# Performance work log

Hardware: AMD Instinct MI355X
Metric: run time of the kernel (lower is better)

## Reference

```python
import jax, jax.numpy as jnp
import numpy as np

B, DX, DY, K, H = 131072, 256, 32, 4, 128
TIMESTEPS = 1000
LR, REG, SW = 0.1, 0.01, 1.0


def setup_inputs() -> dict:
    key = jax.random.key(0)
    ks = jax.random.split(key, 12)
    n = lambda k, shp, s=0.05: (jax.random.normal(k, shp) * s).astype(jnp.float32)
    return {
        "x": jax.random.normal(ks[0], (B, DX), jnp.float32),
        "t": jax.random.randint(ks[1], (B,), 0, K),
        "e_w1": n(ks[2], (DX + DY, H)), "e_b1": jnp.zeros((H,), jnp.float32),
        "e_w2": n(ks[3], (H, H)),       "e_b2": jnp.zeros((H,), jnp.float32),
        "e_w3": n(ks[4], (H, K)),       "e_b3": jnp.zeros((K,), jnp.float32),
        "s_xw": n(ks[5], (DX, H)),      "s_xb": jnp.zeros((H,), jnp.float32),
        "s_yw": n(ks[6], (DY, H)),      "s_yb": jnp.zeros((H,), jnp.float32),
        "s_temb": n(ks[7], (K, H)),
        "s_t1w": n(ks[8], (1, H)),      "s_t1b": jnp.zeros((H,), jnp.float32),
        "s_t2w": n(ks[9], (H, H)),      "s_t2b": jnp.zeros((H,), jnp.float32),
        "tr1w": n(ks[10], (4 * H, H)),  "tr1b": jnp.zeros((H,), jnp.float32),
        "tr2w": n(ks[11], (H, K)),      "tr2b": jnp.zeros((K,), jnp.float32),
        "steps": 20,
    }


def reference(x, t, e_w1, e_b1, e_w2, e_b2, e_w3, e_b3,
              s_xw, s_xb, s_yw, s_yb, s_temb, s_t1w, s_t1b, s_t2w, s_t2b,
              tr1w, tr1b, tr2w, tr2b, steps):
    tc = jnp.maximum(t, 0)                      # clamp_min(0)
    tci = tc[:, None]                           # [B,1] gather index
    valid = (t >= 0).astype(jnp.float32)[:, None]
    tau = jnp.maximum(tc.astype(jnp.float32) / TIMESTEPS, 1e-6)[:, None]  # [B,1]

    # y-independent precomputations (hoisted out of the loop)
    hx_e = x @ e_w1[:DX] + e_b1                 # energy first layer, x part [B,H]
    hx_s = x @ s_xw + s_xb                      # score x_proj [B,H]
    temb = s_temb[tc]                           # t embedding [B,H]
    th = jax.nn.silu(tau @ s_t1w + s_t1b) @ s_t2w + s_t2b  # time_fc [B,H]

    def total_fn(y):
        # EnergyNet: Linear-ReLU-Linear-ReLU-Linear on cat([x,y])
        h1 = jax.nn.relu(hx_e + y @ e_w1[DX:])
        e_all = jax.nn.relu(h1 @ e_w2 + e_b2) @ e_w3 + e_b3          # [B,K]
        e = jnp.take_along_axis(e_all, tci, axis=1)                  # [B,1]
        tot = e + REG * jnp.sum(y * y, axis=1, keepdims=True)
        # ScoreNet trunk on cat([x_proj, y_proj, t_embed, time_fc])
        hy = y @ s_yw + s_yb
        h = jnp.concatenate([hx_s, hy, temb, th], axis=-1)           # [B,4H]
        logits = jax.nn.silu(h @ tr1w + tr1b) @ tr2w + tr2b          # [B,K]
        ce = jax.nn.logsumexp(logits, axis=-1, keepdims=True) - jnp.take_along_axis(logits, tci, axis=1)
        return jnp.sum(tot + SW * ce * valid)

    grad_fn = jax.grad(total_fn)

    def step(carry, _):
        y, done = carry
        g = grad_fn(y)
        done = done | (jnp.sqrt(jnp.sum(g * g)) < 1e-3)  # torch: break before update
        y = jnp.where(done, y, y - LR * g)
        return (y, done), None

    y0 = jnp.zeros((x.shape[0], DY), jnp.float32)
    (y, _), _ = jax.lax.scan(step, (y0, jnp.array(False)), None, length=steps)
    return y
```

## Files before the change

kernel.cpp:

```cpp
#include <hip/hip_runtime.h>
#include <hip/hip_bf16.h>

#define DXc 256
#define DYc 32
#define Kc 4
#define Hc 128
#define LRf 0.1f
#define REGf 0.01f
#define TSTEPS 1000

typedef __attribute__((ext_vector_type(8))) short s8b;
typedef __attribute__((ext_vector_type(4))) float f32x4;

#define MFMA16(a, b, c) __builtin_amdgcn_mfma_f32_16x16x32_bf16((a), (b), (c), 0, 0, 0)

#define MFMA6(A0, A1, A2, B0, B1, B2, acc)      \
    do {                                        \
        acc = MFMA16((A0), (B0), acc);          \
        acc = MFMA16((A0), (B1), acc);          \
        acc = MFMA16((A1), (B0), acc);          \
        acc = MFMA16((A0), (B2), acc);          \
        acc = MFMA16((A1), (B1), acc);          \
        acc = MFMA16((A2), (B0), acc);          \
    } while (0)

__device__ __forceinline__ float hipart(float a) {
    return __uint_as_float(__float_as_uint(a) & 0xffff0000u);
}
__device__ __forceinline__ unsigned hi2(float a, float b) {
    return (__float_as_uint(a) >> 16) | (__float_as_uint(b) & 0xffff0000u);
}
__device__ __forceinline__ void wsplit(float x, unsigned short* __restrict__ h,
                                       unsigned short* __restrict__ l) {
    unsigned u = __float_as_uint(x);
    *h = (unsigned short)(u >> 16);
    float hf = __uint_as_float(u & 0xffff0000u);
    *l = (unsigned short)(__float_as_uint(x - hf) >> 16);
}
__device__ __forceinline__ void wsplit3(float x, unsigned short* __restrict__ p0,
                                        unsigned short* __restrict__ p1,
                                        unsigned short* __restrict__ p2) {
    unsigned u = __float_as_uint(x);
    *p0 = (unsigned short)(u >> 16);
    float r1 = x - __uint_as_float(u & 0xffff0000u);
    unsigned u1 = __float_as_uint(r1);
    *p1 = (unsigned short)(u1 >> 16);
    float r2 = r1 - __uint_as_float(u1 & 0xffff0000u);
    *p2 = (unsigned short)(__float_as_uint(r2) >> 16);
}
__device__ __forceinline__ void split3x8(const float* v, s8b& A0, s8b& A1, s8b& A2) {
    union { s8b s; unsigned u[4]; } P0, P1, P2;
    #pragma unroll
    for (int m = 0; m < 4; ++m) {
        float a = v[2 * m], b = v[2 * m + 1];
        unsigned ua = __float_as_uint(a), ub = __float_as_uint(b);
        P0.u[m] = (ua >> 16) | (ub & 0xffff0000u);
        float ra = a - __uint_as_float(ua & 0xffff0000u);
        float rb = b - __uint_as_float(ub & 0xffff0000u);
        unsigned ura = __float_as_uint(ra), urb = __float_as_uint(rb);
        P1.u[m] = (ura >> 16) | (urb & 0xffff0000u);
        float ra2 = ra - __uint_as_float(ura & 0xffff0000u);
        float rb2 = rb - __uint_as_float(urb & 0xffff0000u);
        P2.u[m] = (__float_as_uint(ra2) >> 16) | (__float_as_uint(rb2) & 0xffff0000u);
    }
    A0 = P0.s; A1 = P1.s; A2 = P2.s;
}
__device__ __forceinline__ void split3pack4(const float* v, uint2& Q0, uint2& Q1, uint2& Q2) {
    float r1[4], r2[4];
    #pragma unroll
    for (int i = 0; i < 4; ++i) {
        r1[i] = v[i] - hipart(v[i]);
        r2[i] = r1[i] - hipart(r1[i]);
    }
    Q0.x = hi2(v[0], v[1]);   Q0.y = hi2(v[2], v[3]);
    Q1.x = hi2(r1[0], r1[1]); Q1.y = hi2(r1[2], r1[3]);
    Q2.x = hi2(r2[0], r2[1]); Q2.y = hi2(r2[2], r2[3]);
}
__device__ __forceinline__ void split2pack4(const float* v, uint2& Q0, uint2& Q1) {
    Q0.x = hi2(v[0], v[1]); Q0.y = hi2(v[2], v[3]);
    float r0 = v[0] - hipart(v[0]), r1 = v[1] - hipart(v[1]);
    float r2 = v[2] - hipart(v[2]), r3 = v[3] - hipart(v[3]);
    Q1.x = hi2(r0, r1); Q1.y = hi2(r2, r3);
}

__global__ __launch_bounds__(256) void setup_kernel(
    const float* __restrict__ e_w1, const float* __restrict__ s_xw,
    const float* __restrict__ s_yw, const float* __restrict__ s_temb,
    const float* __restrict__ s_t1w, const float* __restrict__ s_t1b,
    const float* __restrict__ s_t2w, const float* __restrict__ s_t2b,
    const float* __restrict__ tr1w, const float* __restrict__ tr1b,
    const float* __restrict__ s_xb, const float* __restrict__ s_yb,
    const float* __restrict__ e_w2,
    float* __restrict__ Wcat, float* __restrict__ W1, float* __restrict__ d0,
    unsigned short* __restrict__ W1Tb0, unsigned short* __restrict__ W1Tb1,
    unsigned short* __restrict__ W1Tb2,
    unsigned short* __restrict__ ew2Tb0, unsigned short* __restrict__ ew2Tb1,
    unsigned short* __restrict__ ew2Tb2,
    unsigned short* __restrict__ ew2bh, unsigned short* __restrict__ ew2bl,
    unsigned short* __restrict__ Wdybh, unsigned short* __restrict__ Wdybl)
{
    const int b = blockIdx.x;
    const int t = threadIdx.x;
    if (b < 64) {
        #pragma unroll
        for (int i = 0; i < 2; ++i) {
            int idx = t + 256 * i;
            int k = 4 * b + (idx >> 7);
            int c = idx & 127;
            float acc = 0.f;
            for (int h = 0; h < 128; ++h)
                acc += s_xw[k * 128 + h] * tr1w[h * 128 + c];
            Wcat[k * 256 + 128 + c] = acc;
            Wcat[k * 256 + c] = e_w1[k * 128 + c];
        }
    } else if (b == 64) {
        #pragma unroll
        for (int i = 0; i < 16; ++i) {
            int idx = t + 256 * i;
            int d = idx >> 7, c = idx & 127;
            float acc = 0.f;
            for (int h = 0; h < 128; ++h)
                acc += s_yw[d * 128 + h] * tr1w[(128 + h) * 128 + c];
            W1[d * 256 + 128 + c] = acc;
            wsplit3(acc, &W1Tb0[(128 + c) * 32 + d], &W1Tb1[(128 + c) * 32 + d],
                    &W1Tb2[(128 + c) * 32 + d]);
            wsplit(acc, &Wdybh[d * 256 + c], &Wdybl[d * 256 + c]);
        }
    } else if (b == 65) {
        #pragma unroll
        for (int i = 0; i < 16; ++i) {
            int idx = t + 256 * i;
            int d = idx >> 7, c = idx & 127;
            float v = e_w1[(DXc + d) * 128 + c];
            W1[d * 256 + c] = v;
            wsplit3(v, &W1Tb0[c * 32 + d], &W1Tb1[c * 32 + d], &W1Tb2[c * 32 + d]);
            wsplit(v, &Wdybh[d * 256 + 128 + c], &Wdybl[d * 256 + 128 + c]);
        }
    } else if (b == 66) {
        #pragma unroll
        for (int i = 0; i < 64; ++i) {
            int idx = t + 256 * i;
            int h = idx >> 7, c = idx & 127;
            float v = e_w2[h * 128 + c];
            wsplit3(v, &ew2Tb0[c * 128 + h], &ew2Tb1[c * 128 + h],
                    &ew2Tb2[c * 128 + h]);
            wsplit(v, &ew2bh[h * 128 + c], &ew2bl[h * 128 + c]);
        }
    } else {
        __shared__ float thS[4][128];
        #pragma unroll
        for (int i = 0; i < 2; ++i) {
            int idx = t + 256 * i;
            int tt = idx >> 7, c = idx & 127;
            float tau = (float)tt / (float)TSTEPS;
            if (tau < 1e-6f) tau = 1e-6f;
            float acc = s_t2b[c];
            for (int h = 0; h < 128; ++h) {
                float aa = tau * s_t1w[h] + s_t1b[h];
                float s = 1.f / (1.f + expf(-aa));
                acc += aa * s * s_t2w[h * 128 + c];
            }
            thS[tt][c] = acc;
        }
        __syncthreads();
        #pragma unroll
        for (int i = 0; i < 2; ++i) {
            int idx = t + 256 * i;
            int tt = idx >> 7, c = idx & 127;
            float acc = tr1b[c];
            for (int h = 0; h < 128; ++h) {
                acc += s_temb[tt * 128 + h] * tr1w[(256 + h) * 128 + c];
                acc += thS[tt][h]           * tr1w[(384 + h) * 128 + c];
                acc += s_yb[h]              * tr1w[(128 + h) * 128 + c];
                acc += s_xb[h]              * tr1w[h * 128 + c];
            }
            d0[tt * 128 + c] = acc;
        }
    }
}

__global__ __launch_bounds__(256) void rowpre_kernel(
    const float* __restrict__ x, const int* __restrict__ tin,
    const float* __restrict__ Wcat, const float* __restrict__ e_b1,
    const float* __restrict__ d0,
    float* __restrict__ hxeP, float* __restrict__ cbP)
{
    __shared__ float XsT[64][68];
    __shared__ int tS[64];
    __shared__ float eb1S[128];

    const int t = threadIdx.x;
    const int r0 = blockIdx.x * 64;
    if (t < 64) { int tv = tin[r0 + t]; tS[t] = tv > 0 ? tv : 0; }
    if (t < 128) eb1S[t] = e_b1[t];

    const int rg = t >> 4;
    const int cg = t & 15;
    const int R = rg << 2;

    float acc[4][16];
    #pragma unroll
    for (int rr = 0; rr < 4; ++rr)
        #pragma unroll
        for (int cc = 0; cc < 16; ++cc) acc[rr][cc] = 0.f;

    for (int kc = 0; kc < 4; ++kc) {
        __syncthreads();
        #pragma unroll
        for (int i = 0; i < 4; ++i) {
            int lin = t + 256 * i;
            int rr = lin >> 4;
            int c4 = (lin & 15) << 2;
            float4 v = *(const float4*)&x[(size_t)(r0 + rr) * 256 + kc * 64 + c4];
            XsT[c4 + 0][rr] = v.x;
            XsT[c4 + 1][rr] = v.y;
            XsT[c4 + 2][rr] = v.z;
            XsT[c4 + 3][rr] = v.w;
        }
        __syncthreads();
        #pragma unroll 2
        for (int k = 0; k < 64; ++k) {
            float av[4];
            #pragma unroll
            for (int rr = 0; rr < 4; ++rr) av[rr] = XsT[k][R + rr];
            const float* wrow = &Wcat[(size_t)(kc * 64 + k) * 256 + cg];
            #pragma unroll
            for (int cc = 0; cc < 16; ++cc) {
                float bv = wrow[cc * 16];
                #pragma unroll
                for (int rr = 0; rr < 4; ++rr) acc[rr][cc] += av[rr] * bv;
            }
        }
    }
    #pragma unroll
    for (int cc = 0; cc < 8; ++cc) {
        int c = cg + (cc << 4);
        #pragma unroll
        for (int rr = 0; rr < 4; ++rr)
            hxeP[(size_t)(r0 + R + rr) * 128 + c] = acc[rr][cc] + eb1S[c];
    }
    #pragma unroll
    for (int cc = 8; cc < 16; ++cc) {
        int c = cg + ((cc - 8) << 4);
        #pragma unroll
        for (int rr = 0; rr < 4; ++rr)
            cbP[(size_t)(r0 + R + rr) * 128 + c] = acc[rr][cc] + d0[tS[R + rr] * 128 + c];
    }
}

__global__ __launch_bounds__(256) void iterate_kernel(
    const float* __restrict__ hxeP, const float* __restrict__ cbP,
    const unsigned short* __restrict__ W1Tb0, const unsigned short* __restrict__ W1Tb1,
    const unsigned short* __restrict__ W1Tb2,
    const unsigned short* __restrict__ ew2Tb0, const unsigned short* __restrict__ ew2Tb1,
    const unsigned short* __restrict__ ew2Tb2,
    const unsigned short* __restrict__ ew2bh, const unsigned short* __restrict__ ew2bl,
    const unsigned short* __restrict__ Wdybh, const unsigned short* __restrict__ Wdybl,
    const float* __restrict__ e_w3, const float* __restrict__ tr2w,
    const float* __restrict__ tr2b, const float* __restrict__ e_b2,
    const int* __restrict__ tin, const int* __restrict__ stepsPtr,
    float* __restrict__ yout)
{
    __shared__ __align__(16) unsigned short H1a[32 * 136];
    __shared__ __align__(16) unsigned short H1b[32 * 136];
    __shared__ __align__(16) unsigned short H1c[32 * 136];
    __shared__ __align__(16) unsigned short DAa[32 * 136], DAb[32 * 136];
    __shared__ __align__(16) float U[32 * 140];
    __shared__ __align__(16) float yS[32 * 36];
    __shared__ __align__(16) float tr2wS[2 * 520];
    __shared__ float ew3S[512];
    __shared__ float eb2S[128];
    __shared__ float vSs[32];
    __shared__ int tcS[32];

    const int t = threadIdx.x;
    const int r0 = blockIdx.x * 32;
    const int w = t >> 6;
    const int l = t & 63;
    const int g = l >> 4;
    const int q = l & 15;

    if (t < 32) {
        int tv = tin[r0 + t];
        tcS[t] = tv > 0 ? tv : 0;
        vSs[t] = (tv >= 0) ? 1.f : 0.f;
    }
    if (t < 128) eb2S[t] = e_b2[t];
    for (int i = t; i < 512; i += 256) {
        float wv = tr2w[i];
        ew3S[i] = e_w3[i];
        tr2wS[i] = wv;
        tr2wS[520 + i] = wv;
    }
    for (int i = t; i < 32 * 36; i += 256) yS[i] = 0.f;

    float4 vhc4[4][2];
    {
        const float* src = (w < 2) ? hxeP : cbP;
        const int wb = (w < 2) ? w : (w - 2);
        #pragma unroll
        for (int ci = 0; ci < 4; ++ci)
            #pragma unroll
            for (int ct = 0; ct < 2; ++ct)
                vhc4[ci][ct] = *(const float4*)
                    &src[(size_t)(r0 + ct * 16 + q) * 128 + (wb * 4 + ci) * 16 + g * 4];
    }

    s8b W1A0[4], W1A1[4], W1A2[4];
    #pragma unroll
    for (int ci = 0; ci < 4; ++ci) {
        const int arow = (w * 4 + ci) * 16 + q;
        W1A0[ci] = *(const s8b*)&W1Tb0[arow * 32 + g * 8];
        W1A1[ci] = *(const s8b*)&W1Tb1[arow * 32 + g * 8];
        W1A2[ci] = *(const s8b*)&W1Tb2[arow * 32 + g * 8];
    }

    const float tb0 = tr2b[0], tb1 = tr2b[1], tb2 = tr2b[2], tb3 = tr2b[3];
    const int nsteps = stepsPtr[0];
    const int row8 = t >> 3;
    const int p = t & 7;

    __syncthreads();

    for (int step = 0; step < nsteps; ++step) {
        #pragma unroll
        for (int ct = 0; ct < 2; ++ct) {
            float4 ya = *(const float4*)&yS[(ct * 16 + q) * 36 + g * 8];
            float4 yb = *(const float4*)&yS[(ct * 16 + q) * 36 + g * 8 + 4];
            float yv[8] = {ya.x, ya.y, ya.z, ya.w, yb.x, yb.y, yb.z, yb.w};
            s8b Y0, Y1, Y2;
            split3x8(yv, Y0, Y1, Y2);
            #pragma unroll
            for (int ci = 0; ci < 4; ++ci) {
                f32x4 acc = {0.f, 0.f, 0.f, 0.f};
                MFMA6(W1A0[ci], W1A1[ci], W1A2[ci], Y0, Y1, Y2, acc);
                const float4 vb = vhc4[ci][ct];
                if (w < 2) {
                    float v[4];
                    v[0] = acc[0] + vb.x; v[1] = acc[1] + vb.y;
                    v[2] = acc[2] + vb.z; v[3] = acc[3] + vb.w;
                    #pragma unroll
                    for (int j = 0; j < 4; ++j) v[j] = v[j] > 0.f ? v[j] : 0.f;
                    uint2 Q0, Q1, Q2;
                    split3pack4(v, Q0, Q1, Q2);
                    const int off = (ct * 16 + q) * 136 + (w * 4 + ci) * 16 + g * 4;
                    *(uint2*)&H1a[off] = Q0;
                    *(uint2*)&H1b[off] = Q1;
                    *(uint2*)&H1c[off] = Q2;
                } else {
                    float4 o;
                    o.x = acc[0] + vb.x; o.y = acc[1] + vb.y;
                    o.z = acc[2] + vb.z; o.w = acc[3] + vb.w;
                    const int off = (ct * 16 + q) * 140 + ((w - 2) * 4 + ci) * 16 + g * 4;
                    *(float4*)&U[off] = o;
                }
            }
        }
        __syncthreads();

        {
            float aval[16], sval[16];
            float lg0 = 0.f, lg1 = 0.f, lg2 = 0.f, lg3 = 0.f;
            const int h0 = p << 4;
            const float* ap = &U[row8 * 140 + h0];
            #pragma unroll
            for (int m = 0; m < 4; ++m) {
                float4 v4 = *(const float4*)&ap[m * 4];
                aval[m * 4 + 0] = v4.x; aval[m * 4 + 1] = v4.y;
                aval[m * 4 + 2] = v4.z; aval[m * 4 + 3] = v4.w;
            }
            const float* tw = &tr2wS[(p & 1) * 520];
            #pragma unroll
            for (int hh = 0; hh < 16; ++hh) {
                float a = aval[hh];
                float s = 1.f / (1.f + __expf(-a));
                sval[hh] = s;
                float u = a * s;
                float4 wv4 = *(const float4*)&tw[(h0 + hh) * 4];
                lg0 += u * wv4.x; lg1 += u * wv4.y;
                lg2 += u * wv4.z; lg3 += u * wv4.w;
            }
            #pragma unroll
            for (int m = 1; m < 8; m <<= 1) {
                lg0 += __shfl_xor(lg0, m);
                lg1 += __shfl_xor(lg1, m);
                lg2 += __shfl_xor(lg2, m);
                lg3 += __shfl_xor(lg3, m);
            }
            lg0 += tb0; lg1 += tb1; lg2 += tb2; lg3 += tb3;
            float mx = fmaxf(fmaxf(lg0, lg1), fmaxf(lg2, lg3));
            float e0 = __expf(lg0 - mx), e1 = __expf(lg1 - mx);
            float e2 = __expf(lg2 - mx), e3 = __expf(lg3 - mx);
            float inv = 1.f / (e0 + e1 + e2 + e3);
            int tcr = tcS[row8];
            float vd = vSs[row8];
            float dl0 = (e0 * inv - (tcr == 0 ? 1.f : 0.f)) * vd;
            float dl1 = (e1 * inv - (tcr == 1 ? 1.f : 0.f)) * vd;
            float dl2 = (e2 * inv - (tcr == 2 ? 1.f : 0.f)) * vd;
            float dl3 = (e3 * inv - (tcr == 3 ? 1.f : 0.f)) * vd;
            #pragma unroll
            for (int hh = 0; hh < 16; ++hh) {
                float a = aval[hh], s = sval[hh];
                float4 wv4 = *(const float4*)&tw[(h0 + hh) * 4];
                float du = dl0 * wv4.x + dl1 * wv4.y + dl2 * wv4.z + dl3 * wv4.w;
                aval[hh] = du * s * (1.f + a * (1.f - s));
            }
            #pragma unroll
            for (int m = 0; m < 8; ++m) {
                float a0 = aval[2 * m], a1 = aval[2 * m + 1];
                *(unsigned*)&DAa[row8 * 136 + h0 + 2 * m] = hi2(a0, a1);
                *(unsigned*)&DAb[row8 * 136 + h0 + 2 * m] =
                    hi2(a0 - hipart(a0), a1 - hipart(a1));
            }
        }
        __syncthreads();

        {
            unsigned short* DZh = (unsigned short*)U;
            unsigned short* DZl = DZh + 32 * 136;
            #pragma unroll
            for (int ct = 0; ct < 2; ++ct) {
                s8b Ba[4], Bb[4], Bc[4];
                #pragma unroll
                for (int kc = 0; kc < 4; ++kc) {
                    const int off = (ct * 16 + q) * 136 + kc * 32 + g * 8;
                    Ba[kc] = *(const s8b*)&H1a[off];
                    Bb[kc] = *(const s8b*)&H1b[off];
                    Bc[kc] = *(const s8b*)&H1c[off];
                }
                #pragma unroll
                for (int c2 = 0; c2 < 2; ++c2) {
                    const int ctl = w * 2 + c2;
                    f32x4 acc = {0.f, 0.f, 0.f, 0.f};
                    #pragma unroll
                    for (int kc = 0; kc < 4; ++kc) {
                        const int wo = (ctl * 16 + q) * 128 + kc * 32 + g * 8;
                        s8b A0 = *(const s8b*)&ew2Tb0[wo];
                        s8b A1 = *(const s8b*)&ew2Tb1[wo];
                        s8b A2 = *(const s8b*)&ew2Tb2[wo];
                        MFMA6(A0, A1, A2, Ba[kc], Bb[kc], Bc[kc], acc);
                    }
                    const int cb = ctl * 16 + g * 4;
                    const int smp = ct * 16 + q;
                    const float4 eb = *(const float4*)&eb2S[cb];
                    const int tcr = tcS[smp];
                    float dz[4];
                    dz[0] = (acc[0] + eb.x) > 0.f ? ew3S[(cb + 0) * 4 + tcr] : 0.f;
                    dz[1] = (acc[1] + eb.y) > 0.f ? ew3S[(cb + 1) * 4 + tcr] : 0.f;
                    dz[2] = (acc[2] + eb.z) > 0.f ? ew3S[(cb + 2) * 4 + tcr] : 0.f;
                    dz[3] = (acc[3] + eb.w) > 0.f ? ew3S[(cb + 3) * 4 + tcr] : 0.f;
                    uint2 Q0, Q1;
                    split2pack4(dz, Q0, Q1);
                    const int off = smp * 136 + cb;
                    *(uint2*)&DZh[off] = Q0;
                    *(uint2*)&DZl[off] = Q1;
                }
            }
        }
        __syncthreads();

        {
            const unsigned short* DZh = (const unsigned short*)U;
            const unsigned short* DZl = DZh + 32 * 136;
            #pragma unroll
            for (int ct = 0; ct < 2; ++ct) {
                s8b Bh[4], Bl[4];
                #pragma unroll
                for (int kc = 0; kc < 4; ++kc) {
                    const int off = (ct * 16 + q) * 136 + kc * 32 + g * 8;
                    Bh[kc] = *(const s8b*)&DZh[off];
                    Bl[kc] = *(const s8b*)&DZl[off];
                }
                #pragma unroll
                for (int c2 = 0; c2 < 2; ++c2) {
                    const int htl = w * 2 + c2;
                    f32x4 acc = {0.f, 0.f, 0.f, 0.f};
                    #pragma unroll
                    for (int kc = 0; kc < 4; ++kc) {
                        const int wo = (htl * 16 + q) * 128 + kc * 32 + g * 8;
                        s8b Ah = *(const s8b*)&ew2bh[wo];
                        s8b Al = *(const s8b*)&ew2bl[wo];
                        acc = MFMA16(Ah, Bh[kc], acc);
                        acc = MFMA16(Al, Bh[kc], acc);
                        acc = MFMA16(Ah, Bl[kc], acc);
                    }
                    const int hb = htl * 16 + g * 4;
                    const int smp = ct * 16 + q;
                    const int off = smp * 136 + hb;
                    const uint2 mh = *(const uint2*)&H1a[off];
                    float v[4];
                    v[0] = ((short)(mh.x & 0xffffu) > 0) ? acc[0] : 0.f;
                    v[1] = ((short)(mh.x >> 16)     > 0) ? acc[1] : 0.f;
                    v[2] = ((short)(mh.y & 0xffffu) > 0) ? acc[2] : 0.f;
                    v[3] = ((short)(mh.y >> 16)     > 0) ? acc[3] : 0.f;
                    uint2 Q0, Q1;
                    split2pack4(v, Q0, Q1);
                    *(uint2*)&H1a[off] = Q0;
                    *(uint2*)&H1b[off] = Q1;
                }
            }
        }
        __syncthreads();

        {
            const int dt = w >> 1, st = w & 1;
            f32x4 acc = {0.f, 0.f, 0.f, 0.f};
            #pragma unroll
            for (int kc = 0; kc < 8; ++kc) {
                const int boff = (st * 16 + q) * 136 + (kc & 3) * 32 + g * 8;
                s8b bh, bl;
                if (kc < 4) { bh = *(const s8b*)&DAa[boff]; bl = *(const s8b*)&DAb[boff]; }
                else        { bh = *(const s8b*)&H1a[boff]; bl = *(const s8b*)&H1b[boff]; }
                const int aoff = (dt * 16 + q) * 256 + kc * 32 + g * 8;
                s8b ah = *(const s8b*)&Wdybh[aoff];
                s8b al = *(const s8b*)&Wdybl[aoff];
                acc = MFMA16(ah, bh, acc);
                acc = MFMA16(al, bh, acc);
                acc = MFMA16(ah, bl, acc);
            }
            const int smp = st * 16 + q;
            const int db = dt * 16 + g * 4;
            float4 yv4 = *(const float4*)&yS[smp * 36 + db];
            yv4.x -= LRf * (acc[0] + 2.f * REGf * yv4.x);
            yv4.y -= LRf * (acc[1] + 2.f * REGf * yv4.y);
            yv4.z -= LRf * (acc[2] + 2.f * REGf * yv4.z);
            yv4.w -= LRf * (acc[3] + 2.f * REGf * yv4.w);
            *(float4*)&yS[smp * 36 + db] = yv4;
        }
        __syncthreads();
    }

    {
        const int row = t >> 3;
        const int d4 = (t & 7) * 4;
        float4 o = *(const float4*)&yS[row * 36 + d4];
        *(float4*)&yout[(size_t)(r0 + row) * 32 + d4] = o;
    }
}

extern "C" void kernel_launch(void* const* d_in, const int* in_sizes, int n_in,
                              void* d_out, int out_size, void* d_ws, size_t ws_size,
                              hipStream_t stream)
{
    const float* x      = (const float*)d_in[0];
    const int*   tin    = (const int*)d_in[1];
    const float* e_w1   = (const float*)d_in[2];
    const float* e_b1   = (const float*)d_in[3];
    const float* e_w2   = (const float*)d_in[4];
    const float* e_b2   = (const float*)d_in[5];
    const float* e_w3   = (const float*)d_in[6];
    const float* s_xw   = (const float*)d_in[8];
    const float* s_xb   = (const float*)d_in[9];
    const float* s_yw   = (const float*)d_in[10];
    const float* s_yb   = (const float*)d_in[11];
    const float* s_temb = (const float*)d_in[12];
    const float* s_t1w  = (const float*)d_in[13];
    const float* s_t1b  = (const float*)d_in[14];
    const float* s_t2w  = (const float*)d_in[15];
    const float* s_t2b  = (const float*)d_in[16];
    const float* tr1w   = (const float*)d_in[17];
    const float* tr1b   = (const float*)d_in[18];
    const float* tr2w   = (const float*)d_in[19];
    const float* tr2b   = (const float*)d_in[20];
    const int*   steps  = (const int*)d_in[21];

    const int B = in_sizes[0] / DXc;

    float* ws    = (float*)d_ws;
    float* hxeP  = ws;
    float* cbP   = hxeP + (size_t)B * 128;
    float* Wcat  = cbP  + (size_t)B * 128;
    float* W1    = Wcat + 256 * 256;
    float* d0    = W1   + 32 * 256;

    unsigned short* W1Tb0  = (unsigned short*)(d0 + 4 * 128);
    unsigned short* W1Tb1  = W1Tb0  + 256 * 32;
    unsigned short* W1Tb2  = W1Tb1  + 256 * 32;
    unsigned short* ew2Tb0 = W1Tb2  + 256 * 32;
    unsigned short* ew2Tb1 = ew2Tb0 + 128 * 128;
    unsigned short* ew2Tb2 = ew2Tb1 + 128 * 128;
    unsigned short* ew2bh  = ew2Tb2 + 128 * 128;
    unsigned short* ew2bl  = ew2bh  + 128 * 128;
    unsigned short* Wdybh  = ew2bl  + 128 * 128;
    unsigned short* Wdybl  = Wdybh  + 32 * 256;

    setup_kernel<<<68, 256, 0, stream>>>(e_w1, s_xw, s_yw, s_temb, s_t1w, s_t1b,
                                         s_t2w, s_t2b, tr1w, tr1b, s_xb, s_yb,
                                         e_w2, Wcat, W1, d0,
                                         W1Tb0, W1Tb1, W1Tb2,
                                         ew2Tb0, ew2Tb1, ew2Tb2,
                                         ew2bh, ew2bl, Wdybh, Wdybl);
    rowpre_kernel<<<B / 64, 256, 0, stream>>>(x, tin, Wcat, e_b1, d0, hxeP, cbP);
    iterate_kernel<<<B / 32, 256, 0, stream>>>(hxeP, cbP,
                                               W1Tb0, W1Tb1, W1Tb2,
                                               ew2Tb0, ew2Tb1, ew2Tb2,
                                               ew2bh, ew2bl, Wdybh, Wdybl,
                                               e_w3, tr2w, tr2b, e_b2, tin,
                                               steps, (float*)d_out);
}
```

Measured before the change: 3.485 ms.

## Move row precompute to split-bf16 MFMA and widen iterate blocks to 512 threads

The row precompute GEMM (x times the concatenated energy/score weights) moves from scalar FP32 FMAs to 3-way split bf16 MFMA, with the setup kernel emitting transposed split weights. The iterate kernel goes from 256 to 512 threads per block, so each wave owns fewer column tiles, and the trunk epilogue is restructured to 16 lanes per row. Per-step bias vectors are now reloaded from global memory instead of being held in registers, and tr2w lives in registers instead of shared memory. This trades register pressure and serial per-wave work for more waves, at the cost of extra global loads every step.

```diff
diff --git a/kernel.cpp b/kernel.cpp
--- a/kernel.cpp
+++ b/kernel.cpp
@@ -90,8 +90,9 @@
     const float* __restrict__ s_t2w, const float* __restrict__ s_t2b,
     const float* __restrict__ tr1w, const float* __restrict__ tr1b,
     const float* __restrict__ s_xb, const float* __restrict__ s_yb,
-    const float* __restrict__ e_w2,
-    float* __restrict__ Wcat, float* __restrict__ W1, float* __restrict__ d0,
+    const float* __restrict__ e_w2, float* __restrict__ d0,
+    unsigned short* __restrict__ WcatTb0, unsigned short* __restrict__ WcatTb1,
+    unsigned short* __restrict__ WcatTb2,
     unsigned short* __restrict__ W1Tb0, unsigned short* __restrict__ W1Tb1,
     unsigned short* __restrict__ W1Tb2,
     unsigned short* __restrict__ ew2Tb0, unsigned short* __restrict__ ew2Tb1,
@@ -110,8 +111,11 @@
             float acc = 0.f;
             for (int h = 0; h < 128; ++h)
                 acc += s_xw[k * 128 + h] * tr1w[h * 128 + c];
-            Wcat[k * 256 + 128 + c] = acc;
-            Wcat[k * 256 + c] = e_w1[k * 128 + c];
+            wsplit3(acc, &WcatTb0[(128 + c) * 256 + k], &WcatTb1[(128 + c) * 256 + k],
+                    &WcatTb2[(128 + c) * 256 + k]);
+            float ev = e_w1[k * 128 + c];
+            wsplit3(ev, &WcatTb0[c * 256 + k], &WcatTb1[c * 256 + k],
+                    &WcatTb2[c * 256 + k]);
         }
     } else if (b == 64) {
         #pragma unroll
@@ -121,7 +125,6 @@
             float acc = 0.f;
             for (int h = 0; h < 128; ++h)
                 acc += s_yw[d * 128 + h] * tr1w[(128 + h) * 128 + c];
-            W1[d * 256 + 128 + c] = acc;
             wsplit3(acc, &W1Tb0[(128 + c) * 32 + d], &W1Tb1[(128 + c) * 32 + d],
                     &W1Tb2[(128 + c) * 32 + d]);
             wsplit(acc, &Wdybh[d * 256 + c], &Wdybl[d * 256 + c]);
@@ -132,7 +135,6 @@
             int idx = t + 256 * i;
             int d = idx >> 7, c = idx & 127;
             float v = e_w1[(DXc + d) * 128 + c];
-            W1[d * 256 + c] = v;
             wsplit3(v, &W1Tb0[c * 32 + d], &W1Tb1[c * 32 + d], &W1Tb2[c * 32 + d]);
             wsplit(v, &Wdybh[d * 256 + 128 + c], &Wdybl[d * 256 + 128 + c]);
         }
@@ -181,74 +183,60 @@
 
 __global__ __launch_bounds__(256) void rowpre_kernel(
     const float* __restrict__ x, const int* __restrict__ tin,
-    const float* __restrict__ Wcat, const float* __restrict__ e_b1,
-    const float* __restrict__ d0,
+    const unsigned short* __restrict__ WcatTb0,
+    const unsigned short* __restrict__ WcatTb1,
+    const unsigned short* __restrict__ WcatTb2,
+    const float* __restrict__ e_b1, const float* __restrict__ d0,
     float* __restrict__ hxeP, float* __restrict__ cbP)
 {
-    __shared__ float XsT[64][68];
     __shared__ int tS[64];
-    __shared__ float eb1S[128];
-
     const int t = threadIdx.x;
     const int r0 = blockIdx.x * 64;
+    const int w = t >> 6;
+    const int l = t & 63;
+    const int g = l >> 4, q = l & 15;
     if (t < 64) { int tv = tin[r0 + t]; tS[t] = tv > 0 ? tv : 0; }
-    if (t < 128) eb1S[t] = e_b1[t];
-
-    const int rg = t >> 4;
-    const int cg = t & 15;
-    const int R = rg << 2;
-
-    float acc[4][16];
-    #pragma unroll
-    for (int rr = 0; rr < 4; ++rr)
-        #pragma unroll
-        for (int cc = 0; cc < 16; ++cc) acc[rr][cc] = 0.f;
-
-    for (int kc = 0; kc < 4; ++kc) {
-        __syncthreads();
-        #pragma unroll
-        for (int i = 0; i < 4; ++i) {
-            int lin = t + 256 * i;
-            int rr = lin >> 4;
-            int c4 = (lin & 15) << 2;
-            float4 v = *(const float4*)&x[(size_t)(r0 + rr) * 256 + kc * 64 + c4];
-            XsT[c4 + 0][rr] = v.x;
-            XsT[c4 + 1][rr] = v.y;
-            XsT[c4 + 2][rr] = v.z;
-            XsT[c4 + 3][rr] = v.w;
-        }
-        __syncthreads();
-        #pragma unroll 2
-        for (int k = 0; k < 64; ++k) {
-            float av[4];
-            #pragma unroll
-            for (int rr = 0; rr < 4; ++rr) av[rr] = XsT[k][R + rr];
-            const float* wrow = &Wcat[(size_t)(kc * 64 + k) * 256 + cg];
-            #pragma unroll
-            for (int cc = 0; cc < 16; ++cc) {
-                float bv = wrow[cc * 16];
-                #pragma unroll
-                for (int rr = 0; rr < 4; ++rr) acc[rr][cc] += av[rr] * bv;
-            }
-        }
-    }
-    #pragma unroll
-    for (int cc = 0; cc < 8; ++cc) {
-        int c = cg + (cc << 4);
-        #pragma unroll
-        for (int rr = 0; rr < 4; ++rr)
-            hxeP[(size_t)(r0 + R + rr) * 128 + c] = acc[rr][cc] + eb1S[c];
-    }
-    #pragma unroll
-    for (int cc = 8; cc < 16; ++cc) {
-        int c = cg + ((cc - 8) << 4);
-        #pragma unroll
-        for (int rr = 0; rr < 4; ++rr)
-            cbP[(size_t)(r0 + R + rr) * 128 + c] = acc[rr][cc] + d0[tS[R + rr] * 128 + c];
-    }
-}
-
-__global__ __launch_bounds__(256) void iterate_kernel(
+    __syncthreads();
+
+    for (int st = 0; st < 4; ++st) {
+        const int smp = r0 + st * 16 + q;
+        s8b Xb0[8], Xb1[8], Xb2[8];
+        #pragma unroll
+        for (int kc = 0; kc < 8; ++kc) {
+            const float* xp = &x[(size_t)smp * 256 + kc * 32 + g * 8];
+            float4 xa = *(const float4*)xp;
+            float4 xb = *(const float4*)(xp + 4);
+            float xv[8] = {xa.x, xa.y, xa.z, xa.w, xb.x, xb.y, xb.z, xb.w};
+            split3x8(xv, Xb0[kc], Xb1[kc], Xb2[kc]);
+        }
+        #pragma unroll
+        for (int ci = 0; ci < 4; ++ci) {
+            const int colt = w * 4 + ci;
+            f32x4 acc = {0.f, 0.f, 0.f, 0.f};
+            #pragma unroll
+            for (int kc = 0; kc < 8; ++kc) {
+                const int wo = (colt * 16 + q) * 256 + kc * 32 + g * 8;
+                s8b A0 = *(const s8b*)&WcatTb0[wo];
+                s8b A1 = *(const s8b*)&WcatTb1[wo];
+                s8b A2 = *(const s8b*)&WcatTb2[wo];
+                MFMA6(A0, A1, A2, Xb0[kc], Xb1[kc], Xb2[kc], acc);
+            }
+            const int cb = colt * 16 + g * 4;
+            if (colt < 8) {
+                float4 bv = *(const float4*)&e_b1[cb];
+                float4 o = {acc[0] + bv.x, acc[1] + bv.y, acc[2] + bv.z, acc[3] + bv.w};
+                *(float4*)&hxeP[(size_t)smp * 128 + cb] = o;
+            } else {
+                const int cc = cb - 128;
+                float4 dd = *(const float4*)&d0[tS[st * 16 + q] * 128 + cc];
+                float4 o = {acc[0] + dd.x, acc[1] + dd.y, acc[2] + dd.z, acc[3] + dd.w};
+                *(float4*)&cbP[(size_t)smp * 128 + cc] = o;
+            }
+        }
+    }
+}
+
+__global__ __launch_bounds__(512, 4) void iterate_kernel(
     const float* __restrict__ hxeP, const float* __restrict__ cbP,
     const unsigned short* __restrict__ W1Tb0, const unsigned short* __restrict__ W1Tb1,
     const unsigned short* __restrict__ W1Tb2,
@@ -267,7 +255,6 @@
     __shared__ __align__(16) unsigned short DAa[32 * 136], DAb[32 * 136];
     __shared__ __align__(16) float U[32 * 140];
     __shared__ __align__(16) float yS[32 * 36];
-    __shared__ __align__(16) float tr2wS[2 * 520];
     __shared__ float ew3S[512];
     __shared__ float eb2S[128];
     __shared__ float vSs[32];
@@ -279,6 +266,8 @@
     const int l = t & 63;
     const int g = l >> 4;
     const int q = l & 15;
+    const int row = t >> 4;
+    const int p = t & 15;
 
     if (t < 32) {
         int tv = tin[r0 + t];
@@ -286,39 +275,26 @@
         vSs[t] = (tv >= 0) ? 1.f : 0.f;
     }
     if (t < 128) eb2S[t] = e_b2[t];
-    for (int i = t; i < 512; i += 256) {
-        float wv = tr2w[i];
-        ew3S[i] = e_w3[i];
-        tr2wS[i] = wv;
-        tr2wS[520 + i] = wv;
-    }
-    for (int i = t; i < 32 * 36; i += 256) yS[i] = 0.f;
-
-    float4 vhc4[4][2];
+    ew3S[t] = e_w3[t];
+    for (int i = t; i < 32 * 36; i += 512) yS[i] = 0.f;
+
+    float4 trw4[8];
     {
-        const float* src = (w < 2) ? hxeP : cbP;
-        const int wb = (w < 2) ? w : (w - 2);
-        #pragma unroll
-        for (int ci = 0; ci < 4; ++ci)
-            #pragma unroll
-            for (int ct = 0; ct < 2; ++ct)
-                vhc4[ci][ct] = *(const float4*)
-                    &src[(size_t)(r0 + ct * 16 + q) * 128 + (wb * 4 + ci) * 16 + g * 4];
-    }
-
-    s8b W1A0[4], W1A1[4], W1A2[4];
+        const int h0 = p * 8;
+        #pragma unroll
+        for (int j = 0; j < 8; ++j)
+            trw4[j] = *(const float4*)&tr2w[(h0 + j) * 4];
+    }
+    s8b W1A0[2], W1A1[2], W1A2[2];
     #pragma unroll
-    for (int ci = 0; ci < 4; ++ci) {
-        const int arow = (w * 4 + ci) * 16 + q;
+    for (int ci = 0; ci < 2; ++ci) {
+        const int arow = (2 * w + ci) * 16 + q;
         W1A0[ci] = *(const s8b*)&W1Tb0[arow * 32 + g * 8];
         W1A1[ci] = *(const s8b*)&W1Tb1[arow * 32 + g * 8];
         W1A2[ci] = *(const s8b*)&W1Tb2[arow * 32 + g * 8];
     }
-
     const float tb0 = tr2b[0], tb1 = tr2b[1], tb2 = tr2b[2], tb3 = tr2b[3];
     const int nsteps = stepsPtr[0];
-    const int row8 = t >> 3;
-    const int p = t & 7;
 
     __syncthreads();
 
@@ -331,11 +307,13 @@
             s8b Y0, Y1, Y2;
             split3x8(yv, Y0, Y1, Y2);
             #pragma unroll
-            for (int ci = 0; ci < 4; ++ci) {
+            for (int ci = 0; ci < 2; ++ci) {
+                const int colt = 2 * w + ci;
                 f32x4 acc = {0.f, 0.f, 0.f, 0.f};
                 MFMA6(W1A0[ci], W1A1[ci], W1A2[ci], Y0, Y1, Y2, acc);
-                const float4 vb = vhc4[ci][ct];
-                if (w < 2) {
+                if (w < 4) {
+                    const float4 vb = *(const float4*)
+                        &hxeP[(size_t)(r0 + ct * 16 + q) * 128 + colt * 16 + g * 4];
                     float v[4];
                     v[0] = acc[0] + vb.x; v[1] = acc[1] + vb.y;
                     v[2] = acc[2] + vb.z; v[3] = acc[3] + vb.w;
@@ -343,45 +321,42 @@
                     for (int j = 0; j < 4; ++j) v[j] = v[j] > 0.f ? v[j] : 0.f;
                     uint2 Q0, Q1, Q2;
                     split3pack4(v, Q0, Q1, Q2);
-                    const int off = (ct * 16 + q) * 136 + (w * 4 + ci) * 16 + g * 4;
+                    const int off = (ct * 16 + q) * 136 + colt * 16 + g * 4;
                     *(uint2*)&H1a[off] = Q0;
                     *(uint2*)&H1b[off] = Q1;
                     *(uint2*)&H1c[off] = Q2;
                 } else {
-                    float4 o;
-                    o.x = acc[0] + vb.x; o.y = acc[1] + vb.y;
-                    o.z = acc[2] + vb.z; o.w = acc[3] + vb.w;
-                    const int off = (ct * 16 + q) * 140 + ((w - 2) * 4 + ci) * 16 + g * 4;
-                    *(float4*)&U[off] = o;
+                    const int cc = (colt - 8) * 16 + g * 4;
+                    const float4 vb = *(const float4*)
+                        &cbP[(size_t)(r0 + ct * 16 + q) * 128 + cc];
+                    float4 o = {acc[0] + vb.x, acc[1] + vb.y,
+                                acc[2] + vb.z, acc[3] + vb.w};
+                    *(float4*)&U[(ct * 16 + q) * 140 + cc] = o;
                 }
             }
         }
         __syncthreads();
 
         {
-            float aval[16], sval[16];
+            float aval[8], sval[8];
             float lg0 = 0.f, lg1 = 0.f, lg2 = 0.f, lg3 = 0.f;
-            const int h0 = p << 4;
-            const float* ap = &U[row8 * 140 + h0];
-            #pragma unroll
-            for (int m = 0; m < 4; ++m) {
-                float4 v4 = *(const float4*)&ap[m * 4];
-                aval[m * 4 + 0] = v4.x; aval[m * 4 + 1] = v4.y;
-                aval[m * 4 + 2] = v4.z; aval[m * 4 + 3] = v4.w;
-            }
-            const float* tw = &tr2wS[(p & 1) * 520];
-            #pragma unroll
-            for (int hh = 0; hh < 16; ++hh) {
-                float a = aval[hh];
+            const int h0 = p * 8;
+            const float* ap = &U[row * 140 + h0];
+            float4 v0 = *(const float4*)ap;
+            float4 v1 = *(const float4*)(ap + 4);
+            aval[0] = v0.x; aval[1] = v0.y; aval[2] = v0.z; aval[3] = v0.w;
+            aval[4] = v1.x; aval[5] = v1.y; aval[6] = v1.z; aval[7] = v1.w;
+            #pragma unroll
+            for (int j = 0; j < 8; ++j) {
+                float a = aval[j];
                 float s = 1.f / (1.f + __expf(-a));
-                sval[hh] = s;
+                sval[j] = s;
                 float u = a * s;
-                float4 wv4 = *(const float4*)&tw[(h0 + hh) * 4];
-                lg0 += u * wv4.x; lg1 += u * wv4.y;
-                lg2 += u * wv4.z; lg3 += u * wv4.w;
-            }
-            #pragma unroll
-            for (int m = 1; m < 8; m <<= 1) {
+                lg0 += u * trw4[j].x; lg1 += u * trw4[j].y;
+                lg2 += u * trw4[j].z; lg3 += u * trw4[j].w;
+            }
+            #pragma unroll
+            for (int m = 1; m < 16; m <<= 1) {
                 lg0 += __shfl_xor(lg0, m);
                 lg1 += __shfl_xor(lg1, m);
                 lg2 += __shfl_xor(lg2, m);
@@ -392,69 +367,83 @@
             float e0 = __expf(lg0 - mx), e1 = __expf(lg1 - mx);
             float e2 = __expf(lg2 - mx), e3 = __expf(lg3 - mx);
             float inv = 1.f / (e0 + e1 + e2 + e3);
-            int tcr = tcS[row8];
-            float vd = vSs[row8];
+            int tcr = tcS[row];
+            float vd = vSs[row];
             float dl0 = (e0 * inv - (tcr == 0 ? 1.f : 0.f)) * vd;
             float dl1 = (e1 * inv - (tcr == 1 ? 1.f : 0.f)) * vd;
             float dl2 = (e2 * inv - (tcr == 2 ? 1.f : 0.f)) * vd;
             float dl3 = (e3 * inv - (tcr == 3 ? 1.f : 0.f)) * vd;
             #pragma unroll
-            for (int hh = 0; hh < 16; ++hh) {
-                float a = aval[hh], s = sval[hh];
-                float4 wv4 = *(const float4*)&tw[(h0 + hh) * 4];
-                float du = dl0 * wv4.x + dl1 * wv4.y + dl2 * wv4.z + dl3 * wv4.w;
-                aval[hh] = du * s * (1.f + a * (1.f - s));
-            }
-            #pragma unroll
-            for (int m = 0; m < 8; ++m) {
-                float a0 = aval[2 * m], a1 = aval[2 * m + 1];
-                *(unsigned*)&DAa[row8 * 136 + h0 + 2 * m] = hi2(a0, a1);
-                *(unsigned*)&DAb[row8 * 136 + h0 + 2 * m] =
-                    hi2(a0 - hipart(a0), a1 - hipart(a1));
-            }
+            for (int j = 0; j < 8; ++j) {
+                float a = aval[j], s = sval[j];
+                float du = dl0 * trw4[j].x + dl1 * trw4[j].y
+                         + dl2 * trw4[j].z + dl3 * trw4[j].w;
+                aval[j] = du * s * (1.f + a * (1.f - s));
+            }
+            const int off = row * 136 + h0;
+            uint2 Qh0 = {hi2(aval[0], aval[1]), hi2(aval[2], aval[3])};
+            uint2 Qh1 = {hi2(aval[4], aval[5]), hi2(aval[6], aval[7])};
+            float rl[8];
+            #pragma unroll
+            for (int j = 0; j < 8; ++j) rl[j] = aval[j] - hipart(aval[j]);
+            uint2 Ql0 = {hi2(rl[0], rl[1]), hi2(rl[2], rl[3])};
+            uint2 Ql1 = {hi2(rl[4], rl[5]), hi2(rl[6], rl[7])};
+            *(uint2*)&DAa[off] = Qh0;
+            *(uint2*)&DAa[off + 4] = Qh1;
+            *(uint2*)&DAb[off] = Ql0;
+            *(uint2*)&DAb[off + 4] = Ql1;
         }
         __syncthreads();
 
         {
             unsigned short* DZh = (unsigned short*)U;
             unsigned short* DZl = DZh + 32 * 136;
-            #pragma unroll
-            for (int ct = 0; ct < 2; ++ct) {
-                s8b Ba[4], Bb[4], Bc[4];
-                #pragma unroll
-                for (int kc = 0; kc < 4; ++kc) {
-                    const int off = (ct * 16 + q) * 136 + kc * 32 + g * 8;
-                    Ba[kc] = *(const s8b*)&H1a[off];
-                    Bb[kc] = *(const s8b*)&H1b[off];
-                    Bc[kc] = *(const s8b*)&H1c[off];
-                }
-                #pragma unroll
-                for (int c2 = 0; c2 < 2; ++c2) {
-                    const int ctl = w * 2 + c2;
-                    f32x4 acc = {0.f, 0.f, 0.f, 0.f};
-                    #pragma unroll
-                    for (int kc = 0; kc < 4; ++kc) {
-                        const int wo = (ctl * 16 + q) * 128 + kc * 32 + g * 8;
-                        s8b A0 = *(const s8b*)&ew2Tb0[wo];
-                        s8b A1 = *(const s8b*)&ew2Tb1[wo];
-                        s8b A2 = *(const s8b*)&ew2Tb2[wo];
-                        MFMA6(A0, A1, A2, Ba[kc], Bb[kc], Bc[kc], acc);
-                    }
-                    const int cb = ctl * 16 + g * 4;
-                    const int smp = ct * 16 + q;
-                    const float4 eb = *(const float4*)&eb2S[cb];
-                    const int tcr = tcS[smp];
-                    float dz[4];
-                    dz[0] = (acc[0] + eb.x) > 0.f ? ew3S[(cb + 0) * 4 + tcr] : 0.f;
-                    dz[1] = (acc[1] + eb.y) > 0.f ? ew3S[(cb + 1) * 4 + tcr] : 0.f;
-                    dz[2] = (acc[2] + eb.z) > 0.f ? ew3S[(cb + 2) * 4 + tcr] : 0.f;
-                    dz[3] = (acc[3] + eb.w) > 0.f ? ew3S[(cb + 3) * 4 + tcr] : 0.f;
-                    uint2 Q0, Q1;
-                    split2pack4(dz, Q0, Q1);
-                    const int off = smp * 136 + cb;
-                    *(uint2*)&DZh[off] = Q0;
-                    *(uint2*)&DZl[off] = Q1;
-                }
+            f32x4 acc0 = {0.f, 0.f, 0.f, 0.f};
+            f32x4 acc1 = {0.f, 0.f, 0.f, 0.f};
+            #pragma unroll
+            for (int kc = 0; kc < 4; ++kc) {
+                const int b0 = q * 136 + kc * 32 + g * 8;
+                const int b1 = (16 + q) * 136 + kc * 32 + g * 8;
+                s8b B0a = *(const s8b*)&H1a[b0];
+                s8b B0b = *(const s8b*)&H1b[b0];
+                s8b B0c = *(const s8b*)&H1c[b0];
+                s8b B1a = *(const s8b*)&H1a[b1];
+                s8b B1b = *(const s8b*)&H1b[b1];
+                s8b B1c = *(const s8b*)&H1c[b1];
+                const int wo = (w * 16 + q) * 128 + kc * 32 + g * 8;
+                s8b A0 = *(const s8b*)&ew2Tb0[wo];
+                s8b A1 = *(const s8b*)&ew2Tb1[wo];
+                s8b A2 = *(const s8b*)&ew2Tb2[wo];
+                MFMA6(A0, A1, A2, B0a, B0b, B0c, acc0);
+                MFMA6(A0, A1, A2, B1a, B1b, B1c, acc1);
+            }
+            const int cb = w * 16 + g * 4;
+            const float4 eb = *(const float4*)&eb2S[cb];
+            {
+                const int smp = q;
+                const int tcr = tcS[smp];
+                float dz[4];
+                dz[0] = (acc0[0] + eb.x) > 0.f ? ew3S[(cb + 0) * 4 + tcr] : 0.f;
+                dz[1] = (acc0[1] + eb.y) > 0.f ? ew3S[(cb + 1) * 4 + tcr] : 0.f;
+                dz[2] = (acc0[2] + eb.z) > 0.f ? ew3S[(cb + 2) * 4 + tcr] : 0.f;
+                dz[3] = (acc0[3] + eb.w) > 0.f ? ew3S[(cb + 3) * 4 + tcr] : 0.f;
+                uint2 Q0, Q1;
+                split2pack4(dz, Q0, Q1);
+                *(uint2*)&DZh[smp * 136 + cb] = Q0;
+                *(uint2*)&DZl[smp * 136 + cb] = Q1;
+            }
+            {
+                const int smp = 16 + q;
+                const int tcr = tcS[smp];
+                float dz[4];
+                dz[0] = (acc1[0] + eb.x) > 0.f ? ew3S[(cb + 0) * 4 + tcr] : 0.f;
+                dz[1] = (acc1[1] + eb.y) > 0.f ? ew3S[(cb + 1) * 4 + tcr] : 0.f;
+                dz[2] = (acc1[2] + eb.z) > 0.f ? ew3S[(cb + 2) * 4 + tcr] : 0.f;
+                dz[3] = (acc1[3] + eb.w) > 0.f ? ew3S[(cb + 3) * 4 + tcr] : 0.f;
+                uint2 Q0, Q1;
+                split2pack4(dz, Q0, Q1);
+                *(uint2*)&DZh[smp * 136 + cb] = Q0;
+                *(uint2*)&DZl[smp * 136 + cb] = Q1;
             }
         }
         __syncthreads();
@@ -462,47 +451,57 @@
         {
             const unsigned short* DZh = (const unsigned short*)U;
             const unsigned short* DZl = DZh + 32 * 136;
-            #pragma unroll
-            for (int ct = 0; ct < 2; ++ct) {
-                s8b Bh[4], Bl[4];
-                #pragma unroll
-                for (int kc = 0; kc < 4; ++kc) {
-                    const int off = (ct * 16 + q) * 136 + kc * 32 + g * 8;
-                    Bh[kc] = *(const s8b*)&DZh[off];
-                    Bl[kc] = *(const s8b*)&DZl[off];
-                }
-                #pragma unroll
-                for (int c2 = 0; c2 < 2; ++c2) {
-                    const int htl = w * 2 + c2;
-                    f32x4 acc = {0.f, 0.f, 0.f, 0.f};
-                    #pragma unroll
-                    for (int kc = 0; kc < 4; ++kc) {
-                        const int wo = (htl * 16 + q) * 128 + kc * 32 + g * 8;
-                        s8b Ah = *(const s8b*)&ew2bh[wo];
-                        s8b Al = *(const s8b*)&ew2bl[wo];
-                        acc = MFMA16(Ah, Bh[kc], acc);
-                        acc = MFMA16(Al, Bh[kc], acc);
-                        acc = MFMA16(Ah, Bl[kc], acc);
-                    }
-                    const int hb = htl * 16 + g * 4;
-                    const int smp = ct * 16 + q;
-                    const int off = smp * 136 + hb;
-                    const uint2 mh = *(const uint2*)&H1a[off];
-                    float v[4];
-                    v[0] = ((short)(mh.x & 0xffffu) > 0) ? acc[0] : 0.f;
-                    v[1] = ((short)(mh.x >> 16)     > 0) ? acc[1] : 0.f;
-                    v[2] = ((short)(mh.y & 0xffffu) > 0) ? acc[2] : 0.f;
-                    v[3] = ((short)(mh.y >> 16)     > 0) ? acc[3] : 0.f;
-                    uint2 Q0, Q1;
-                    split2pack4(v, Q0, Q1);
-                    *(uint2*)&H1a[off] = Q0;
-                    *(uint2*)&H1b[off] = Q1;
-                }
+            f32x4 acc0 = {0.f, 0.f, 0.f, 0.f};
+            f32x4 acc1 = {0.f, 0.f, 0.f, 0.f};
+            #pragma unroll
+            for (int kc = 0; kc < 4; ++kc) {
+                const int b0 = q * 136 + kc * 32 + g * 8;
+                const int b1 = (16 + q) * 136 + kc * 32 + g * 8;
+                s8b B0h = *(const s8b*)&DZh[b0];
+                s8b B0l = *(const s8b*)&DZl[b0];
+                s8b B1h = *(const s8b*)&DZh[b1];
+                s8b B1l = *(const s8b*)&DZl[b1];
+                const int wo = (w * 16 + q) * 128 + kc * 32 + g * 8;
+                s8b Ah = *(const s8b*)&ew2bh[wo];
+                s8b Al = *(const s8b*)&ew2bl[wo];
+                acc0 = MFMA16(Ah, B0h, acc0);
+                acc0 = MFMA16(Al, B0h, acc0);
+                acc0 = MFMA16(Ah, B0l, acc0);
+                acc1 = MFMA16(Ah, B1h, acc1);
+                acc1 = MFMA16(Al, B1h, acc1);
+                acc1 = MFMA16(Ah, B1l, acc1);
+            }
+            const int hb = w * 16 + g * 4;
+            {
+                const int off = q * 136 + hb;
+                const uint2 mh = *(const uint2*)&H1a[off];
+                float v[4];
+                v[0] = ((short)(mh.x & 0xffffu) > 0) ? acc0[0] : 0.f;
+                v[1] = ((short)(mh.x >> 16)     > 0) ? acc0[1] : 0.f;
+                v[2] = ((short)(mh.y & 0xffffu) > 0) ? acc0[2] : 0.f;
+                v[3] = ((short)(mh.y >> 16)     > 0) ? acc0[3] : 0.f;
+                uint2 Q0, Q1;
+                split2pack4(v, Q0, Q1);
+                *(uint2*)&H1a[off] = Q0;
+                *(uint2*)&H1b[off] = Q1;
+            }
+            {
+                const int off = (16 + q) * 136 + hb;
+                const uint2 mh = *(const uint2*)&H1a[off];
+                float v[4];
+                v[0] = ((short)(mh.x & 0xffffu) > 0) ? acc1[0] : 0.f;
+                v[1] = ((short)(mh.x >> 16)     > 0) ? acc1[1] : 0.f;
+                v[2] = ((short)(mh.y & 0xffffu) > 0) ? acc1[2] : 0.f;
+                v[3] = ((short)(mh.y >> 16)     > 0) ? acc1[3] : 0.f;
+                uint2 Q0, Q1;
+                split2pack4(v, Q0, Q1);
+                *(uint2*)&H1a[off] = Q0;
+                *(uint2*)&H1b[off] = Q1;
             }
         }
         __syncthreads();
 
-        {
+        if (w < 4) {
             const int dt = w >> 1, st = w & 1;
             f32x4 acc = {0.f, 0.f, 0.f, 0.f};
             #pragma unroll
@@ -531,10 +530,10 @@
     }
 
     {
-        const int row = t >> 3;
-        const int d4 = (t & 7) * 4;
-        float4 o = *(const float4*)&yS[row * 36 + d4];
-        *(float4*)&yout[(size_t)(r0 + row) * 32 + d4] = o;
+        const int orow = t >> 4;
+        const int d2 = (t & 15) * 2;
+        *(float2*)&yout[(size_t)(r0 + orow) * 32 + d2] =
+            *(const float2*)&yS[orow * 36 + d2];
     }
 }
 
@@ -566,32 +565,35 @@
 
     const int B = in_sizes[0] / DXc;
 
-    float* ws    = (float*)d_ws;
-    float* hxeP  = ws;
-    float* cbP   = hxeP + (size_t)B * 128;
-    float* Wcat  = cbP  + (size_t)B * 128;
-    float* W1    = Wcat + 256 * 256;
-    float* d0    = W1   + 32 * 256;
-
-    unsigned short* W1Tb0  = (unsigned short*)(d0 + 4 * 128);
-    unsigned short* W1Tb1  = W1Tb0  + 256 * 32;
-    unsigned short* W1Tb2  = W1Tb1  + 256 * 32;
-    unsigned short* ew2Tb0 = W1Tb2  + 256 * 32;
-    unsigned short* ew2Tb1 = ew2Tb0 + 128 * 128;
-    unsigned short* ew2Tb2 = ew2Tb1 + 128 * 128;
-    unsigned short* ew2bh  = ew2Tb2 + 128 * 128;
-    unsigned short* ew2bl  = ew2bh  + 128 * 128;
-    unsigned short* Wdybh  = ew2bl  + 128 * 128;
-    unsigned short* Wdybl  = Wdybh  + 32 * 256;
+    float* ws   = (float*)d_ws;
+    float* hxeP = ws;
+    float* cbP  = hxeP + (size_t)B * 128;
+    float* d0   = cbP  + (size_t)B * 128;
+
+    unsigned short* W1Tb0   = (unsigned short*)(d0 + 4 * 128);
+    unsigned short* W1Tb1   = W1Tb0   + 256 * 32;
+    unsigned short* W1Tb2   = W1Tb1   + 256 * 32;
+    unsigned short* ew2Tb0  = W1Tb2   + 256 * 32;
+    unsigned short* ew2Tb1  = ew2Tb0  + 128 * 128;
+    unsigned short* ew2Tb2  = ew2Tb1  + 128 * 128;
+    unsigned short* ew2bh   = ew2Tb2  + 128 * 128;
+    unsigned short* ew2bl   = ew2bh   + 128 * 128;
+    unsigned short* Wdybh   = ew2bl   + 128 * 128;
+    unsigned short* Wdybl   = Wdybh   + 32 * 256;
+    unsigned short* WcatTb0 = Wdybl   + 32 * 256;
+    unsigned short* WcatTb1 = WcatTb0 + 256 * 256;
+    unsigned short* WcatTb2 = WcatTb1 + 256 * 256;
 
     setup_kernel<<<68, 256, 0, stream>>>(e_w1, s_xw, s_yw, s_temb, s_t1w, s_t1b,
                                          s_t2w, s_t2b, tr1w, tr1b, s_xb, s_yb,
-                                         e_w2, Wcat, W1, d0,
+                                         e_w2, d0,
+                                         WcatTb0, WcatTb1, WcatTb2,
                                          W1Tb0, W1Tb1, W1Tb2,
                                          ew2Tb0, ew2Tb1, ew2Tb2,
                                          ew2bh, ew2bl, Wdybh, Wdybl);
-    rowpre_kernel<<<B / 64, 256, 0, stream>>>(x, tin, Wcat, e_b1, d0, hxeP, cbP);
-    iterate_kernel<<<B / 32, 256, 0, stream>>>(hxeP, cbP,
+    rowpre_kernel<<<B / 64, 256, 0, stream>>>(x, tin, WcatTb0, WcatTb1, WcatTb2,
+                                              e_b1, d0, hxeP, cbP);
+    iterate_kernel<<<B / 32, 512, 0, stream>>>(hxeP, cbP,
                                                W1Tb0, W1Tb1, W1Tb2,
                                                ew2Tb0, ew2Tb1, ew2Tb2,
                                                ew2bh, ew2bl, Wdybh, Wdybl,
```

After: 4.324 ms. 24.1% more time.
